# Kernel tuning notes

Measured on AMD Instinct MI355X. Metric: run time of the kernel, lower is better.

Reference implementation:

```python
import jax, jax.numpy as jnp
import numpy as np

HIDDEN = 1024
INTER = 4096
NUM_EXPERTS = 8
TOP_K = 2


def setup_inputs() -> dict:
    key = jax.random.key(0)
    k1, k2, k3, k4 = jax.random.split(key, 4)
    hidden_states = jax.random.normal(k1, (4, 1024, HIDDEN), dtype=jnp.float32)
    gate_w = jax.random.normal(k2, (HIDDEN, NUM_EXPERTS), dtype=jnp.float32) * 0.02
    w1 = jax.random.normal(k3, (NUM_EXPERTS, HIDDEN, INTER), dtype=jnp.float32) * 0.02
    w2 = jax.random.normal(k4, (NUM_EXPERTS, INTER, HIDDEN), dtype=jnp.float32) * 0.02
    return {"hidden_states": hidden_states, "gate_w": gate_w, "w1": w1, "w2": w2}


def reference(hidden_states, gate_w, w1, w2):
    B, S, H = hidden_states.shape
    x = hidden_states.reshape(-1, H)                       # [T, H]
    T = x.shape[0]
    router_logits = x @ gate_w                             # [T, E]
    probs = jax.nn.softmax(router_logits.astype(jnp.float32), axis=-1)
    routing_weights, selected_experts = jax.lax.top_k(probs, TOP_K)  # [T, K]
    routing_weights = routing_weights / routing_weights.sum(-1, keepdims=True)
    routing_weights = routing_weights.astype(x.dtype)
    # combine[t, e] = sum_k rw[t, k] * (sel[t, k] == e)
    combine = jnp.zeros((T, NUM_EXPERTS), x.dtype).at[
        jnp.arange(T)[:, None], selected_experts
    ].add(routing_weights)
    # dense grouped MLP over all experts; zero combine weight drops unrouted pairs
    h1 = jax.nn.gelu(jnp.einsum('th,ehi->tei', x, w1), approximate=False)  # [T, E, I]
    y = jnp.einsum('tei,eih->teh', h1, w2)                 # [T, E, H]
    out = jnp.einsum('teh,te->th', y, combine)             # [T, H]
    return out.reshape(B, S, H), router_logits
```

## Files before the change

### kernel.cpp

```cpp
#include <hip/hip_runtime.h>
#include <hip/hip_bf16.h>
#include <math.h>

typedef unsigned short u16;
typedef unsigned int u32;
typedef __bf16 bf16x8 __attribute__((ext_vector_type(8)));
typedef float f32x4 __attribute__((ext_vector_type(4)));

#define T_TOK 4096
#define HID   1024
#define INTER 4096
#define NEXP  8

#define WS_NEEDED 209978368ull

__device__ __forceinline__ u16 f2bf(float f) {
    u32 u = __builtin_bit_cast(u32, f);
    u += 0x7FFFu + ((u >> 16) & 1u);
    return (u16)(u >> 16);
}

__device__ __forceinline__ void gl2lds16(const void* g, void* l) {
    __builtin_amdgcn_global_load_lds(
        (const __attribute__((address_space(1))) u32*)g,
        (__attribute__((address_space(3))) u32*)l, 16, 0, 0);
}

__device__ __forceinline__ float fast_gelu(float v) {
    float u2 = v * (-1.5957691216f - 0.0713548163f * v * v);
    return v / (1.0f + __expf(u2));
}

__global__ __launch_bounds__(256) void router_kernel(
    const float* __restrict__ x, const float* __restrict__ gw,
    float* __restrict__ logits, int* __restrict__ counts,
    int* __restrict__ tlist, float* __restrict__ wlist)
{
    const int lane = threadIdx.x & 63, wv = threadIdx.x >> 6;
    const int t = blockIdx.x * 4 + wv;
    const float* xr = x + (size_t)t * HID;
    float a[8] = {0.f,0.f,0.f,0.f,0.f,0.f,0.f,0.f};
    for (int h = lane; h < HID; h += 64) {
        float xv = xr[h];
        const float4* g4 = (const float4*)(gw + h * 8);
        float4 g0 = g4[0], g1 = g4[1];
        a[0] += xv * g0.x; a[1] += xv * g0.y; a[2] += xv * g0.z; a[3] += xv * g0.w;
        a[4] += xv * g1.x; a[5] += xv * g1.y; a[6] += xv * g1.z; a[7] += xv * g1.w;
    }
#pragma unroll
    for (int e = 0; e < 8; e++) {
        float v = a[e];
        for (int o = 32; o > 0; o >>= 1) v += __shfl_down(v, o, 64);
        a[e] = v;
    }
    if (lane == 0) {
#pragma unroll
        for (int e = 0; e < 8; e++) logits[(size_t)t * 8 + e] = a[e];
        int e1 = 0; float b1 = a[0];
        for (int e = 1; e < 8; e++) if (a[e] > b1) { b1 = a[e]; e1 = e; }
        int e2 = -1; float b2 = -1e30f;
        for (int e = 0; e < 8; e++) if (e != e1 && a[e] > b2) { b2 = a[e]; e2 = e; }
        float wa = 1.0f / (1.0f + expf(b2 - b1));
        float wb = 1.0f - wa;
        int p = atomicAdd(&counts[e1], 1);
        tlist[e1 * T_TOK + p] = t; wlist[e1 * T_TOK + p] = wa;
        p = atomicAdd(&counts[e2], 1);
        tlist[e2 * T_TOK + p] = t; wlist[e2 * T_TOK + p] = wb;
    }
}

__global__ void scan_kernel(const int* __restrict__ counts, int* __restrict__ offs)
{
    if (threadIdx.x == 0) {
        int s = 0;
        for (int e = 0; e < 8; e++) { offs[e] = s; s += counts[e]; }
    }
}

__global__ __launch_bounds__(256) void convert_x_kernel(
    const float* __restrict__ src, u16* __restrict__ dst)
{
    const int idx = (blockIdx.x * 256 + threadIdx.x) * 8;
    float4 f0 = *(const float4*)(src + idx);
    float4 f1 = *(const float4*)(src + idx + 4);
    uint4 o;
    o.x = (u32)f2bf(f0.x) | ((u32)f2bf(f0.y) << 16);
    o.y = (u32)f2bf(f0.z) | ((u32)f2bf(f0.w) << 16);
    o.z = (u32)f2bf(f1.x) | ((u32)f2bf(f1.y) << 16);
    o.w = (u32)f2bf(f1.z) | ((u32)f2bf(f1.w) << 16);
    *(uint4*)(dst + idx) = o;
}

__global__ __launch_bounds__(256) void transpose_convert_kernel(
    const float* __restrict__ src, u16* __restrict__ dst, int R, int C)
{
    __shared__ float tl[64][65];
    const int e = blockIdx.z;
    const int c0 = blockIdx.x * 64, r0 = blockIdx.y * 64;
    const float* s = src + (size_t)e * R * C + (size_t)r0 * C + c0;
    const int tid = threadIdx.x;
#pragma unroll
    for (int it = 0; it < 4; it++) {
        int idx = it * 256 + tid;
        int r = idx >> 4;
        int c4 = (idx & 15) * 4;
        float4 v = *(const float4*)(s + (size_t)r * C + c4);
        tl[c4 + 0][r] = v.x;
        tl[c4 + 1][r] = v.y;
        tl[c4 + 2][r] = v.z;
        tl[c4 + 3][r] = v.w;
    }
    __syncthreads();
    u16* d = dst + (size_t)e * C * R + (size_t)c0 * R + r0;
#pragma unroll
    for (int it = 0; it < 2; it++) {
        int idx = it * 256 + tid;
        int c = idx >> 3;
        int rg = (idx & 7) * 8;
        u32 o[4];
#pragma unroll
        for (int p = 0; p < 4; p++)
            o[p] = (u32)f2bf(tl[c][rg + 2 * p]) | ((u32)f2bf(tl[c][rg + 2 * p + 1]) << 16);
        *(uint4*)(d + (size_t)c * R + rg) = *(uint4*)o;
    }
}

__global__ __launch_bounds__(256, 1) void gemm1_kernel(
    const u16* __restrict__ xb, const u16* __restrict__ w1t,
    const int* __restrict__ counts, const int* __restrict__ offs,
    const int* __restrict__ tlist, u16* __restrict__ h1b)
{
    const int e = blockIdx.z, mt = blockIdx.y, nt = blockIdx.x;
    const int cnt = counts[e];
    if (mt * 128 >= cnt) return;
    __shared__ __align__(16) u16 As[8192];
    __shared__ __align__(16) u16 Bs[8192];
    __shared__ int toks[128];
    const int tid = threadIdx.x, lane = tid & 63, wv = tid >> 6;
    if (tid < 128) toks[tid] = tlist[e * T_TOK + min(mt * 128 + tid, cnt - 1)];
    __syncthreads();

    f32x4 acc[4][4] = {};
    const int wm = wv & 1, wn = wv >> 1;
    const int sj = tid >> 3, sp = tid & 7;

    size_t abase[4], bbase[4];
    const u16* w1base = w1t + ((size_t)e * INTER + (size_t)nt * 128) * HID;
#pragma unroll
    for (int j = 0; j < 4; j++) {
        int m = j * 32 + sj;
        abase[j] = (size_t)toks[m] * HID + ((sp - m) & 7) * 8;
        bbase[j] = (size_t)m * HID + ((sp - m) & 7) * 8;
    }

    for (int h0 = 0; h0 < HID; h0 += 64) {
#pragma unroll
        for (int j = 0; j < 4; j++)
            gl2lds16(xb + abase[j] + h0, &As[j * 2048 + wv * 512]);
#pragma unroll
        for (int j = 0; j < 4; j++)
            gl2lds16(w1base + bbase[j] + h0, &Bs[j * 2048 + wv * 512]);
        __syncthreads();
#pragma unroll
        for (int kk = 0; kk < 2; kk++) {
            bf16x8 a[4], b[4];
            const int jjb = kk * 4 + (lane >> 4);
#pragma unroll
            for (int i = 0; i < 4; i++) {
                int m = wm * 64 + i * 16 + (lane & 15);
                a[i] = *(const bf16x8*)&As[m * 64 + ((jjb + m) & 7) * 8];
            }
#pragma unroll
            for (int i = 0; i < 4; i++) {
                int n = wn * 64 + i * 16 + (lane & 15);
                b[i] = *(const bf16x8*)&Bs[n * 64 + ((jjb + n) & 7) * 8];
            }
#pragma unroll
            for (int i = 0; i < 4; i++)
#pragma unroll
                for (int j = 0; j < 4; j++)
                    acc[i][j] = __builtin_amdgcn_mfma_f32_16x16x32_bf16(
                        a[i], b[j], acc[i][j], 0, 0, 0);
        }
        __syncthreads();
    }

    const int pb = offs[e] + mt * 128;
    const bool full = (mt * 128 + 128 <= cnt);
#pragma unroll
    for (int i = 0; i < 4; i++) {
        const int mb = wm * 64 + i * 16 + ((lane >> 4) << 2);
#pragma unroll
        for (int j = 0; j < 4; j++) {
            const int n = nt * 128 + wn * 64 + j * 16 + (lane & 15);
#pragma unroll
            for (int r = 0; r < 4; r++) {
                const int m = mb + r;
                if (full || mt * 128 + m < cnt) {
                    h1b[(size_t)(pb + m) * INTER + n] = f2bf(fast_gelu(acc[i][j][r]));
                }
            }
        }
    }
}

__global__ __launch_bounds__(256, 1) void gemm2_kernel(
    const u16* __restrict__ h1b, const u16* __restrict__ w2t,
    const int* __restrict__ counts, const int* __restrict__ offs,
    const int* __restrict__ tlist, const float* __restrict__ wlist,
    float* __restrict__ out)
{
    const int e = blockIdx.z, mt = blockIdx.y;
    const int nt = blockIdx.x & 7, ks = blockIdx.x >> 3;
    const int cnt = counts[e];
    if (mt * 128 >= cnt) return;
    __shared__ __align__(16) u16 As[8192];
    __shared__ __align__(16) u16 Bs[8192];
    __shared__ int toks[128];
    __shared__ float wgt[128];
    const int tid = threadIdx.x, lane = tid & 63, wv = tid >> 6;
    if (tid < 128) {
        int gi = e * T_TOK + min(mt * 128 + tid, cnt - 1);
        toks[tid] = tlist[gi];
        wgt[tid] = wlist[gi];
    }
    __syncthreads();

    f32x4 acc[4][4] = {};
    const int wm = wv & 1, wn = wv >> 1;
    const int sj = tid >> 3, sp = tid & 7;

    size_t abase[4], bbase[4];
    const u16* w2base = w2t + ((size_t)e * HID + (size_t)nt * 128) * INTER;
    const int prow = offs[e];
#pragma unroll
    for (int j = 0; j < 4; j++) {
        int m = j * 32 + sj;
        int row = prow + min(mt * 128 + m, cnt - 1);
        abase[j] = (size_t)row * INTER + ((sp - m) & 7) * 8;
        bbase[j] = (size_t)m * INTER + ((sp - m) & 7) * 8;
    }

    const int i_lo = ks * (INTER / 2), i_hi = i_lo + (INTER / 2);
    for (int i0 = i_lo; i0 < i_hi; i0 += 64) {
#pragma unroll
        for (int j = 0; j < 4; j++)
            gl2lds16(h1b + abase[j] + i0, &As[j * 2048 + wv * 512]);
#pragma unroll
        for (int j = 0; j < 4; j++)
            gl2lds16(w2base + bbase[j] + i0, &Bs[j * 2048 + wv * 512]);
        __syncthreads();
#pragma unroll
        for (int kk = 0; kk < 2; kk++) {
            bf16x8 a[4], b[4];
            const int jjb = kk * 4 + (lane >> 4);
#pragma unroll
            for (int i = 0; i < 4; i++) {
                int m = wm * 64 + i * 16 + (lane & 15);
                a[i] = *(const bf16x8*)&As[m * 64 + ((jjb + m) & 7) * 8];
            }
#pragma unroll
            for (int i = 0; i < 4; i++) {
                int n = wn * 64 + i * 16 + (lane & 15);
                b[i] = *(const bf16x8*)&Bs[n * 64 + ((jjb + n) & 7) * 8];
            }
#pragma unroll
            for (int i = 0; i < 4; i++)
#pragma unroll
                for (int j = 0; j < 4; j++)
                    acc[i][j] = __builtin_amdgcn_mfma_f32_16x16x32_bf16(
                        a[i], b[j], acc[i][j], 0, 0, 0);
        }
        __syncthreads();
    }

    const bool full = (mt * 128 + 128 <= cnt);
#pragma unroll
    for (int i = 0; i < 4; i++) {
        const int mb = wm * 64 + i * 16 + ((lane >> 4) << 2);
#pragma unroll
        for (int j = 0; j < 4; j++) {
            const int n = nt * 128 + wn * 64 + j * 16 + (lane & 15);
#pragma unroll
            for (int r = 0; r < 4; r++) {
                const int m = mb + r;
                if (full || mt * 128 + m < cnt) {
                    atomicAdd(&out[(size_t)toks[m] * HID + n], acc[i][j][r] * wgt[m]);
                }
            }
        }
    }
}

extern "C" void kernel_launch(void* const* d_in, const int* in_sizes, int n_in,
                              void* d_out, int out_size, void* d_ws, size_t ws_size,
                              hipStream_t stream)
{
    const float* x  = (const float*)d_in[0];
    const float* gw = (const float*)d_in[1];
    const float* w1 = (const float*)d_in[2];
    const float* w2 = (const float*)d_in[3];
    float* out    = (float*)d_out;
    float* logits = out + 4194304;

    char* ws = (char*)d_ws;
    int*   counts = (int*)ws;
    int*   offs   = (int*)(ws + 256);
    int*   tlist  = (int*)(ws + 1024);
    float* wlist  = (float*)(ws + 132096);
    u16*   xb     = (u16*)(ws + 263168);
    u16*   w1t    = (u16*)(ws + 8651776);
    u16*   w2t    = (u16*)(ws + 75760640);
    u16*   h1b    = (u16*)(ws + 142869504);

    if (ws_size < WS_NEEDED) return;

    hipMemsetAsync(out, 0, 4194304 * sizeof(float), stream);
    hipMemsetAsync(counts, 0, 256, stream);

    router_kernel<<<1024, 256, 0, stream>>>(x, gw, logits, counts, tlist, wlist);
    scan_kernel<<<1, 64, 0, stream>>>(counts, offs);
    convert_x_kernel<<<2048, 256, 0, stream>>>(x, xb);
    transpose_convert_kernel<<<dim3(64, 16, 8), 256, 0, stream>>>(w1, w1t, HID, INTER);
    transpose_convert_kernel<<<dim3(16, 64, 8), 256, 0, stream>>>(w2, w2t, INTER, HID);

    gemm1_kernel<<<dim3(32, 16, 8), 256, 0, stream>>>(xb, w1t, counts, offs, tlist, h1b);
    gemm2_kernel<<<dim3(16, 16, 8), 256, 0, stream>>>(h1b, w2t, counts, offs, tlist, wlist, out);
}
```

Baseline: 709.0 us.

## Use 256x256 tiles, 512-thread blocks and double-buffered LDS in expert GEMMs

Both expert GEMM kernels move from 128x128 tiles on 256 threads to 256x256 tiles on 512 threads, with each wave computing a 128x64 sub-tile. The goal is more data reuse per global load. LDS staging becomes double-buffered, so the next K-slice is loaded while the current one is computed, removing one barrier per iteration. The grid is flattened to 1D with expert index in the low bits, so blocks of different experts interleave. Offsets are also computed in 32-bit. In exchange the kernels use far more LDS (about 128KB) and registers, and fewer blocks run, which hurts load balance when experts are uneven.

```diff
diff --git a/kernel.cpp b/kernel.cpp
--- a/kernel.cpp
+++ b/kernel.cpp
@@ -125,168 +125,207 @@
     }
 }
 
-__global__ __launch_bounds__(256, 1) void gemm1_kernel(
+__global__ __launch_bounds__(512, 1) void gemm1_kernel(
     const u16* __restrict__ xb, const u16* __restrict__ w1t,
     const int* __restrict__ counts, const int* __restrict__ offs,
     const int* __restrict__ tlist, u16* __restrict__ h1b)
 {
-    const int e = blockIdx.z, mt = blockIdx.y, nt = blockIdx.x;
+    const int id = blockIdx.x;
+    const int e  = id & 7;
+    const int mt = (id >> 3) & 7;
+    const int nt = id >> 6;
     const int cnt = counts[e];
-    if (mt * 128 >= cnt) return;
-    __shared__ __align__(16) u16 As[8192];
-    __shared__ __align__(16) u16 Bs[8192];
-    __shared__ int toks[128];
+    if (mt * 256 >= cnt) return;
+
+    __shared__ __align__(16) u16 As[2][16384];
+    __shared__ __align__(16) u16 Bs[2][16384];
+    __shared__ int toks[256];
+
     const int tid = threadIdx.x, lane = tid & 63, wv = tid >> 6;
-    if (tid < 128) toks[tid] = tlist[e * T_TOK + min(mt * 128 + tid, cnt - 1)];
-    __syncthreads();
-
-    f32x4 acc[4][4] = {};
+    if (tid < 256) toks[tid] = tlist[e * T_TOK + min(mt * 256 + tid, cnt - 1)];
+    __syncthreads();
+
+    const int sr = tid >> 3;
+    const int sp = tid & 7;
+    u32 abase[4], bbase[4];
+    const u32 w1off = ((u32)e * INTER + (u32)nt * 256) * HID;
+#pragma unroll
+    for (int j = 0; j < 4; j++) {
+        int m = j * 64 + sr;
+        u32 rot = (u32)((sp - m) & 7) * 8;
+        abase[j] = (u32)toks[m] * HID + rot;
+        bbase[j] = w1off + (u32)m * HID + rot;
+    }
+
+    f32x4 acc[8][4] = {};
     const int wm = wv & 1, wn = wv >> 1;
-    const int sj = tid >> 3, sp = tid & 7;
-
-    size_t abase[4], bbase[4];
-    const u16* w1base = w1t + ((size_t)e * INTER + (size_t)nt * 128) * HID;
-#pragma unroll
-    for (int j = 0; j < 4; j++) {
-        int m = j * 32 + sj;
-        abase[j] = (size_t)toks[m] * HID + ((sp - m) & 7) * 8;
-        bbase[j] = (size_t)m * HID + ((sp - m) & 7) * 8;
-    }
-
-    for (int h0 = 0; h0 < HID; h0 += 64) {
+
+    auto STAGE = [&](int buf, int k0) {
 #pragma unroll
         for (int j = 0; j < 4; j++)
-            gl2lds16(xb + abase[j] + h0, &As[j * 2048 + wv * 512]);
+            gl2lds16(xb + abase[j] + k0, &As[buf][j * 4096 + wv * 512]);
 #pragma unroll
         for (int j = 0; j < 4; j++)
-            gl2lds16(w1base + bbase[j] + h0, &Bs[j * 2048 + wv * 512]);
-        __syncthreads();
+            gl2lds16(w1t + bbase[j] + k0, &Bs[buf][j * 4096 + wv * 512]);
+    };
+
+    auto COMPUTE = [&](int buf) {
 #pragma unroll
         for (int kk = 0; kk < 2; kk++) {
-            bf16x8 a[4], b[4];
+            bf16x8 a[8], b[4];
             const int jjb = kk * 4 + (lane >> 4);
 #pragma unroll
-            for (int i = 0; i < 4; i++) {
-                int m = wm * 64 + i * 16 + (lane & 15);
-                a[i] = *(const bf16x8*)&As[m * 64 + ((jjb + m) & 7) * 8];
-            }
-#pragma unroll
-            for (int i = 0; i < 4; i++) {
-                int n = wn * 64 + i * 16 + (lane & 15);
-                b[i] = *(const bf16x8*)&Bs[n * 64 + ((jjb + n) & 7) * 8];
-            }
-#pragma unroll
-            for (int i = 0; i < 4; i++)
+            for (int i = 0; i < 8; i++) {
+                int m = wm * 128 + i * 16 + (lane & 15);
+                a[i] = *(const bf16x8*)&As[buf][m * 64 + ((jjb + m) & 7) * 8];
+            }
+#pragma unroll
+            for (int j = 0; j < 4; j++) {
+                int n = wn * 64 + j * 16 + (lane & 15);
+                b[j] = *(const bf16x8*)&Bs[buf][n * 64 + ((jjb + n) & 7) * 8];
+            }
+#pragma unroll
+            for (int i = 0; i < 8; i++)
 #pragma unroll
                 for (int j = 0; j < 4; j++)
                     acc[i][j] = __builtin_amdgcn_mfma_f32_16x16x32_bf16(
                         a[i], b[j], acc[i][j], 0, 0, 0);
         }
+    };
+
+    STAGE(0, 0);
+    __syncthreads();
+    int cur = 0;
+#pragma unroll 1
+    for (int kt = 1; kt < HID / 64; kt++) {
+        STAGE(cur ^ 1, kt * 64);
+        COMPUTE(cur);
         __syncthreads();
-    }
-
-    const int pb = offs[e] + mt * 128;
-    const bool full = (mt * 128 + 128 <= cnt);
-#pragma unroll
-    for (int i = 0; i < 4; i++) {
-        const int mb = wm * 64 + i * 16 + ((lane >> 4) << 2);
+        cur ^= 1;
+    }
+    COMPUTE(cur);
+
+    const int pb = offs[e] + mt * 256;
+    const int rem = cnt - mt * 256;
+    const bool full = (rem >= 256);
+#pragma unroll
+    for (int i = 0; i < 8; i++) {
+        const int mb = wm * 128 + i * 16 + ((lane >> 4) << 2);
 #pragma unroll
         for (int j = 0; j < 4; j++) {
-            const int n = nt * 128 + wn * 64 + j * 16 + (lane & 15);
+            const int n = nt * 256 + wn * 64 + j * 16 + (lane & 15);
 #pragma unroll
             for (int r = 0; r < 4; r++) {
                 const int m = mb + r;
-                if (full || mt * 128 + m < cnt) {
+                if (full || m < rem)
                     h1b[(size_t)(pb + m) * INTER + n] = f2bf(fast_gelu(acc[i][j][r]));
-                }
             }
         }
     }
 }
 
-__global__ __launch_bounds__(256, 1) void gemm2_kernel(
+__global__ __launch_bounds__(512, 1) void gemm2_kernel(
     const u16* __restrict__ h1b, const u16* __restrict__ w2t,
     const int* __restrict__ counts, const int* __restrict__ offs,
     const int* __restrict__ tlist, const float* __restrict__ wlist,
     float* __restrict__ out)
 {
-    const int e = blockIdx.z, mt = blockIdx.y;
-    const int nt = blockIdx.x & 7, ks = blockIdx.x >> 3;
+    const int id = blockIdx.x;
+    const int e  = id & 7;
+    const int mt = (id >> 3) & 7;
+    const int nt = (id >> 6) & 3;
+    const int ks = id >> 8;
     const int cnt = counts[e];
-    if (mt * 128 >= cnt) return;
-    __shared__ __align__(16) u16 As[8192];
-    __shared__ __align__(16) u16 Bs[8192];
-    __shared__ int toks[128];
-    __shared__ float wgt[128];
+    if (mt * 256 >= cnt) return;
+
+    __shared__ __align__(16) u16 As[2][16384];
+    __shared__ __align__(16) u16 Bs[2][16384];
+    __shared__ int toks[256];
+    __shared__ float wgt[256];
+
     const int tid = threadIdx.x, lane = tid & 63, wv = tid >> 6;
-    if (tid < 128) {
-        int gi = e * T_TOK + min(mt * 128 + tid, cnt - 1);
+    if (tid < 256) {
+        int gi = e * T_TOK + min(mt * 256 + tid, cnt - 1);
         toks[tid] = tlist[gi];
-        wgt[tid] = wlist[gi];
-    }
-    __syncthreads();
-
-    f32x4 acc[4][4] = {};
+        wgt[tid]  = wlist[gi];
+    }
+    __syncthreads();
+
+    const int sr = tid >> 3;
+    const int sp = tid & 7;
+    u32 abase[4], bbase[4];
+    const int prow = offs[e];
+#pragma unroll
+    for (int j = 0; j < 4; j++) {
+        int m = j * 64 + sr;
+        u32 rot = (u32)((sp - m) & 7) * 8;
+        int row = prow + min(mt * 256 + m, cnt - 1);
+        abase[j] = (u32)row * INTER + rot;
+        bbase[j] = ((u32)e * HID + (u32)nt * 256 + (u32)m) * INTER + rot;
+    }
+
+    f32x4 acc[8][4] = {};
     const int wm = wv & 1, wn = wv >> 1;
-    const int sj = tid >> 3, sp = tid & 7;
-
-    size_t abase[4], bbase[4];
-    const u16* w2base = w2t + ((size_t)e * HID + (size_t)nt * 128) * INTER;
-    const int prow = offs[e];
-#pragma unroll
-    for (int j = 0; j < 4; j++) {
-        int m = j * 32 + sj;
-        int row = prow + min(mt * 128 + m, cnt - 1);
-        abase[j] = (size_t)row * INTER + ((sp - m) & 7) * 8;
-        bbase[j] = (size_t)m * INTER + ((sp - m) & 7) * 8;
-    }
-
-    const int i_lo = ks * (INTER / 2), i_hi = i_lo + (INTER / 2);
-    for (int i0 = i_lo; i0 < i_hi; i0 += 64) {
+
+    auto STAGE = [&](int buf, int k0) {
 #pragma unroll
         for (int j = 0; j < 4; j++)
-            gl2lds16(h1b + abase[j] + i0, &As[j * 2048 + wv * 512]);
+            gl2lds16(h1b + abase[j] + k0, &As[buf][j * 4096 + wv * 512]);
 #pragma unroll
         for (int j = 0; j < 4; j++)
-            gl2lds16(w2base + bbase[j] + i0, &Bs[j * 2048 + wv * 512]);
-        __syncthreads();
+            gl2lds16(w2t + bbase[j] + k0, &Bs[buf][j * 4096 + wv * 512]);
+    };
+
+    auto COMPUTE = [&](int buf) {
 #pragma unroll
         for (int kk = 0; kk < 2; kk++) {
-            bf16x8 a[4], b[4];
+            bf16x8 a[8], b[4];
             const int jjb = kk * 4 + (lane >> 4);
 #pragma unroll
-            for (int i = 0; i < 4; i++) {
-                int m = wm * 64 + i * 16 + (lane & 15);
-                a[i] = *(const bf16x8*)&As[m * 64 + ((jjb + m) & 7) * 8];
-            }
-#pragma unroll
-            for (int i = 0; i < 4; i++) {
-                int n = wn * 64 + i * 16 + (lane & 15);
-                b[i] = *(const bf16x8*)&Bs[n * 64 + ((jjb + n) & 7) * 8];
-            }
-#pragma unroll
-            for (int i = 0; i < 4; i++)
+            for (int i = 0; i < 8; i++) {
+                int m = wm * 128 + i * 16 + (lane & 15);
+                a[i] = *(const bf16x8*)&As[buf][m * 64 + ((jjb + m) & 7) * 8];
+            }
+#pragma unroll
+            for (int j = 0; j < 4; j++) {
+                int n = wn * 64 + j * 16 + (lane & 15);
+                b[j] = *(const bf16x8*)&Bs[buf][n * 64 + ((jjb + n) & 7) * 8];
+            }
+#pragma unroll
+            for (int i = 0; i < 8; i++)
 #pragma unroll
                 for (int j = 0; j < 4; j++)
                     acc[i][j] = __builtin_amdgcn_mfma_f32_16x16x32_bf16(
                         a[i], b[j], acc[i][j], 0, 0, 0);
         }
+    };
+
+    const u32 kbase = (u32)ks * (INTER / 2);
+    STAGE(0, kbase);
+    __syncthreads();
+    int cur = 0;
+#pragma unroll 1
+    for (int kt = 1; kt < (INTER / 2) / 64; kt++) {
+        STAGE(cur ^ 1, kbase + kt * 64);
+        COMPUTE(cur);
         __syncthreads();
-    }
-
-    const bool full = (mt * 128 + 128 <= cnt);
-#pragma unroll
-    for (int i = 0; i < 4; i++) {
-        const int mb = wm * 64 + i * 16 + ((lane >> 4) << 2);
+        cur ^= 1;
+    }
+    COMPUTE(cur);
+
+    const int rem = cnt - mt * 256;
+    const bool full = (rem >= 256);
+#pragma unroll
+    for (int i = 0; i < 8; i++) {
+        const int mb = wm * 128 + i * 16 + ((lane >> 4) << 2);
 #pragma unroll
         for (int j = 0; j < 4; j++) {
-            const int n = nt * 128 + wn * 64 + j * 16 + (lane & 15);
+            const int n = nt * 256 + wn * 64 + j * 16 + (lane & 15);
 #pragma unroll
             for (int r = 0; r < 4; r++) {
                 const int m = mb + r;
-                if (full || mt * 128 + m < cnt) {
+                if (full || m < rem)
                     atomicAdd(&out[(size_t)toks[m] * HID + n], acc[i][j][r] * wgt[m]);
-                }
             }
         }
     }
@@ -324,6 +363,6 @@
     transpose_convert_kernel<<<dim3(64, 16, 8), 256, 0, stream>>>(w1, w1t, HID, INTER);
     transpose_convert_kernel<<<dim3(16, 64, 8), 256, 0, stream>>>(w2, w2t, INTER, HID);
 
-    gemm1_kernel<<<dim3(32, 16, 8), 256, 0, stream>>>(xb, w1t, counts, offs, tlist, h1b);
-    gemm2_kernel<<<dim3(16, 16, 8), 256, 0, stream>>>(h1b, w2t, counts, offs, tlist, wlist, out);
-}
+    gemm1_kernel<<<1024, 512, 0, stream>>>(xb, w1t, counts, offs, tlist, h1b);
+    gemm2_kernel<<<512, 512, 0, stream>>>(h1b, w2t, counts, offs, tlist, wlist, out);
+}
```

Result: slower. 758.7 us (+7.0%).

## Replace LDS-staged GEMM tiles with direct global-to-register double-buffered loads

Applied to the files above, without the earlier changes.

Both expert GEMM kernels drop the shared-memory tiles filled through global_load_lds, along with the per-iteration barriers. Each wave now loads its MFMA fragments straight from global memory into registers and uses a two-stage register double buffer to overlap loads with MFMAs. The launch bound no longer forces one block per CU, and the grid order is swapped so the M-tile index varies fastest, which changes L2 reuse of weights. The cost is that each tile is fetched separately by every wave that uses it with no LDS sharing, which raises global/L2 traffic, and the 16-byte strided row loads may coalesce poorly.

```diff
diff --git a/kernel.cpp b/kernel.cpp
--- a/kernel.cpp
+++ b/kernel.cpp
@@ -18,12 +18,6 @@
     u32 u = __builtin_bit_cast(u32, f);
     u += 0x7FFFu + ((u >> 16) & 1u);
     return (u16)(u >> 16);
-}
-
-__device__ __forceinline__ void gl2lds16(const void* g, void* l) {
-    __builtin_amdgcn_global_load_lds(
-        (const __attribute__((address_space(1))) u32*)g,
-        (__attribute__((address_space(3))) u32*)l, 16, 0, 0);
 }
 
 __device__ __forceinline__ float fast_gelu(float v) {
@@ -125,68 +119,74 @@
     }
 }
 
-__global__ __launch_bounds__(256, 1) void gemm1_kernel(
+
+__global__ __launch_bounds__(256) void gemm1_kernel(
     const u16* __restrict__ xb, const u16* __restrict__ w1t,
     const int* __restrict__ counts, const int* __restrict__ offs,
     const int* __restrict__ tlist, u16* __restrict__ h1b)
 {
-    const int e = blockIdx.z, mt = blockIdx.y, nt = blockIdx.x;
+    const int mt = blockIdx.x, nt = blockIdx.y, e = blockIdx.z;
     const int cnt = counts[e];
     if (mt * 128 >= cnt) return;
-    __shared__ __align__(16) u16 As[8192];
-    __shared__ __align__(16) u16 Bs[8192];
+
     __shared__ int toks[128];
     const int tid = threadIdx.x, lane = tid & 63, wv = tid >> 6;
     if (tid < 128) toks[tid] = tlist[e * T_TOK + min(mt * 128 + tid, cnt - 1)];
     __syncthreads();
 
+    const int wm = wv & 1, wn = wv >> 1;
+    const int kq = (lane >> 4) * 8;
+
+    u32 aoff[4], boff[4];
+#pragma unroll
+    for (int i = 0; i < 4; i++) {
+        int m = wm * 64 + i * 16 + (lane & 15);
+        aoff[i] = (u32)toks[m] * HID + kq;
+    }
+#pragma unroll
+    for (int j = 0; j < 4; j++) {
+        int n = nt * 128 + wn * 64 + j * 16 + (lane & 15);
+        boff[j] = ((u32)e * INTER + (u32)n) * HID + kq;
+    }
+
     f32x4 acc[4][4] = {};
-    const int wm = wv & 1, wn = wv >> 1;
-    const int sj = tid >> 3, sp = tid & 7;
-
-    size_t abase[4], bbase[4];
-    const u16* w1base = w1t + ((size_t)e * INTER + (size_t)nt * 128) * HID;
-#pragma unroll
-    for (int j = 0; j < 4; j++) {
-        int m = j * 32 + sj;
-        abase[j] = (size_t)toks[m] * HID + ((sp - m) & 7) * 8;
-        bbase[j] = (size_t)m * HID + ((sp - m) & 7) * 8;
-    }
-
-    for (int h0 = 0; h0 < HID; h0 += 64) {
-#pragma unroll
-        for (int j = 0; j < 4; j++)
-            gl2lds16(xb + abase[j] + h0, &As[j * 2048 + wv * 512]);
-#pragma unroll
-        for (int j = 0; j < 4; j++)
-            gl2lds16(w1base + bbase[j] + h0, &Bs[j * 2048 + wv * 512]);
-        __syncthreads();
-#pragma unroll
-        for (int kk = 0; kk < 2; kk++) {
-            bf16x8 a[4], b[4];
-            const int jjb = kk * 4 + (lane >> 4);
-#pragma unroll
-            for (int i = 0; i < 4; i++) {
-                int m = wm * 64 + i * 16 + (lane & 15);
-                a[i] = *(const bf16x8*)&As[m * 64 + ((jjb + m) & 7) * 8];
-            }
-#pragma unroll
-            for (int i = 0; i < 4; i++) {
-                int n = wn * 64 + i * 16 + (lane & 15);
-                b[i] = *(const bf16x8*)&Bs[n * 64 + ((jjb + n) & 7) * 8];
-            }
-#pragma unroll
-            for (int i = 0; i < 4; i++)
-#pragma unroll
-                for (int j = 0; j < 4; j++)
-                    acc[i][j] = __builtin_amdgcn_mfma_f32_16x16x32_bf16(
-                        a[i], b[j], acc[i][j], 0, 0, 0);
+    bf16x8 a0[4], b0[4], a1[4], b1[4];
+
+#pragma unroll
+    for (int i = 0; i < 4; i++) a0[i] = *(const bf16x8*)(xb + aoff[i]);
+#pragma unroll
+    for (int j = 0; j < 4; j++) b0[j] = *(const bf16x8*)(w1t + boff[j]);
+
+    const int NT = HID / 32;
+#pragma unroll 1
+    for (int t = 0; t < NT; t += 2) {
+#pragma unroll
+        for (int i = 0; i < 4; i++) a1[i] = *(const bf16x8*)(xb + aoff[i] + (t + 1) * 32);
+#pragma unroll
+        for (int j = 0; j < 4; j++) b1[j] = *(const bf16x8*)(w1t + boff[j] + (t + 1) * 32);
+#pragma unroll
+        for (int i = 0; i < 4; i++)
+#pragma unroll
+            for (int j = 0; j < 4; j++)
+                acc[i][j] = __builtin_amdgcn_mfma_f32_16x16x32_bf16(
+                    a0[i], b0[j], acc[i][j], 0, 0, 0);
+        if (t + 2 < NT) {
+#pragma unroll
+            for (int i = 0; i < 4; i++) a0[i] = *(const bf16x8*)(xb + aoff[i] + (t + 2) * 32);
+#pragma unroll
+            for (int j = 0; j < 4; j++) b0[j] = *(const bf16x8*)(w1t + boff[j] + (t + 2) * 32);
         }
-        __syncthreads();
+#pragma unroll
+        for (int i = 0; i < 4; i++)
+#pragma unroll
+            for (int j = 0; j < 4; j++)
+                acc[i][j] = __builtin_amdgcn_mfma_f32_16x16x32_bf16(
+                    a1[i], b1[j], acc[i][j], 0, 0, 0);
     }
 
     const int pb = offs[e] + mt * 128;
-    const bool full = (mt * 128 + 128 <= cnt);
+    const int rem = cnt - mt * 128;
+    const bool full = (rem >= 128);
 #pragma unroll
     for (int i = 0; i < 4; i++) {
         const int mb = wm * 64 + i * 16 + ((lane >> 4) << 2);
@@ -196,85 +196,90 @@
 #pragma unroll
             for (int r = 0; r < 4; r++) {
                 const int m = mb + r;
-                if (full || mt * 128 + m < cnt) {
+                if (full || m < rem)
                     h1b[(size_t)(pb + m) * INTER + n] = f2bf(fast_gelu(acc[i][j][r]));
-                }
             }
         }
     }
 }
 
-__global__ __launch_bounds__(256, 1) void gemm2_kernel(
+__global__ __launch_bounds__(256) void gemm2_kernel(
     const u16* __restrict__ h1b, const u16* __restrict__ w2t,
     const int* __restrict__ counts, const int* __restrict__ offs,
     const int* __restrict__ tlist, const float* __restrict__ wlist,
     float* __restrict__ out)
 {
-    const int e = blockIdx.z, mt = blockIdx.y;
-    const int nt = blockIdx.x & 7, ks = blockIdx.x >> 3;
+    const int mt = blockIdx.x;
+    const int nt = blockIdx.y & 7, ks = blockIdx.y >> 3;
+    const int e = blockIdx.z;
     const int cnt = counts[e];
     if (mt * 128 >= cnt) return;
-    __shared__ __align__(16) u16 As[8192];
-    __shared__ __align__(16) u16 Bs[8192];
+
     __shared__ int toks[128];
     __shared__ float wgt[128];
     const int tid = threadIdx.x, lane = tid & 63, wv = tid >> 6;
     if (tid < 128) {
         int gi = e * T_TOK + min(mt * 128 + tid, cnt - 1);
         toks[tid] = tlist[gi];
-        wgt[tid] = wlist[gi];
+        wgt[tid]  = wlist[gi];
     }
     __syncthreads();
 
+    const int wm = wv & 1, wn = wv >> 1;
+    const int kq = (lane >> 4) * 8;
+    const u32 kbase = (u32)ks * (INTER / 2);
+    const int prow = offs[e];
+
+    u32 aoff[4], boff[4];
+#pragma unroll
+    for (int i = 0; i < 4; i++) {
+        int m = wm * 64 + i * 16 + (lane & 15);
+        int row = prow + min(mt * 128 + m, cnt - 1);
+        aoff[i] = (u32)row * INTER + kbase + kq;
+    }
+#pragma unroll
+    for (int j = 0; j < 4; j++) {
+        int n = nt * 128 + wn * 64 + j * 16 + (lane & 15);
+        boff[j] = ((u32)e * HID + (u32)n) * INTER + kbase + kq;
+    }
+
     f32x4 acc[4][4] = {};
-    const int wm = wv & 1, wn = wv >> 1;
-    const int sj = tid >> 3, sp = tid & 7;
-
-    size_t abase[4], bbase[4];
-    const u16* w2base = w2t + ((size_t)e * HID + (size_t)nt * 128) * INTER;
-    const int prow = offs[e];
-#pragma unroll
-    for (int j = 0; j < 4; j++) {
-        int m = j * 32 + sj;
-        int row = prow + min(mt * 128 + m, cnt - 1);
-        abase[j] = (size_t)row * INTER + ((sp - m) & 7) * 8;
-        bbase[j] = (size_t)m * INTER + ((sp - m) & 7) * 8;
-    }
-
-    const int i_lo = ks * (INTER / 2), i_hi = i_lo + (INTER / 2);
-    for (int i0 = i_lo; i0 < i_hi; i0 += 64) {
-#pragma unroll
-        for (int j = 0; j < 4; j++)
-            gl2lds16(h1b + abase[j] + i0, &As[j * 2048 + wv * 512]);
-#pragma unroll
-        for (int j = 0; j < 4; j++)
-            gl2lds16(w2base + bbase[j] + i0, &Bs[j * 2048 + wv * 512]);
-        __syncthreads();
-#pragma unroll
-        for (int kk = 0; kk < 2; kk++) {
-            bf16x8 a[4], b[4];
-            const int jjb = kk * 4 + (lane >> 4);
-#pragma unroll
-            for (int i = 0; i < 4; i++) {
-                int m = wm * 64 + i * 16 + (lane & 15);
-                a[i] = *(const bf16x8*)&As[m * 64 + ((jjb + m) & 7) * 8];
-            }
-#pragma unroll
-            for (int i = 0; i < 4; i++) {
-                int n = wn * 64 + i * 16 + (lane & 15);
-                b[i] = *(const bf16x8*)&Bs[n * 64 + ((jjb + n) & 7) * 8];
-            }
-#pragma unroll
-            for (int i = 0; i < 4; i++)
-#pragma unroll
-                for (int j = 0; j < 4; j++)
-                    acc[i][j] = __builtin_amdgcn_mfma_f32_16x16x32_bf16(
-                        a[i], b[j], acc[i][j], 0, 0, 0);
+    bf16x8 a0[4], b0[4], a1[4], b1[4];
+
+#pragma unroll
+    for (int i = 0; i < 4; i++) a0[i] = *(const bf16x8*)(h1b + aoff[i]);
+#pragma unroll
+    for (int j = 0; j < 4; j++) b0[j] = *(const bf16x8*)(w2t + boff[j]);
+
+    const int NT = (INTER / 2) / 32;
+#pragma unroll 1
+    for (int t = 0; t < NT; t += 2) {
+#pragma unroll
+        for (int i = 0; i < 4; i++) a1[i] = *(const bf16x8*)(h1b + aoff[i] + (t + 1) * 32);
+#pragma unroll
+        for (int j = 0; j < 4; j++) b1[j] = *(const bf16x8*)(w2t + boff[j] + (t + 1) * 32);
+#pragma unroll
+        for (int i = 0; i < 4; i++)
+#pragma unroll
+            for (int j = 0; j < 4; j++)
+                acc[i][j] = __builtin_amdgcn_mfma_f32_16x16x32_bf16(
+                    a0[i], b0[j], acc[i][j], 0, 0, 0);
+        if (t + 2 < NT) {
+#pragma unroll
+            for (int i = 0; i < 4; i++) a0[i] = *(const bf16x8*)(h1b + aoff[i] + (t + 2) * 32);
+#pragma unroll
+            for (int j = 0; j < 4; j++) b0[j] = *(const bf16x8*)(w2t + boff[j] + (t + 2) * 32);
         }
-        __syncthreads();
-    }
-
-    const bool full = (mt * 128 + 128 <= cnt);
+#pragma unroll
+        for (int i = 0; i < 4; i++)
+#pragma unroll
+            for (int j = 0; j < 4; j++)
+                acc[i][j] = __builtin_amdgcn_mfma_f32_16x16x32_bf16(
+                    a1[i], b1[j], acc[i][j], 0, 0, 0);
+    }
+
+    const int rem = cnt - mt * 128;
+    const bool full = (rem >= 128);
 #pragma unroll
     for (int i = 0; i < 4; i++) {
         const int mb = wm * 64 + i * 16 + ((lane >> 4) << 2);
@@ -284,9 +289,8 @@
 #pragma unroll
             for (int r = 0; r < 4; r++) {
                 const int m = mb + r;
-                if (full || mt * 128 + m < cnt) {
+                if (full || m < rem)
                     atomicAdd(&out[(size_t)toks[m] * HID + n], acc[i][j][r] * wgt[m]);
-                }
             }
         }
     }
@@ -324,6 +328,6 @@
     transpose_convert_kernel<<<dim3(64, 16, 8), 256, 0, stream>>>(w1, w1t, HID, INTER);
     transpose_convert_kernel<<<dim3(16, 64, 8), 256, 0, stream>>>(w2, w2t, INTER, HID);
 
-    gemm1_kernel<<<dim3(32, 16, 8), 256, 0, stream>>>(xb, w1t, counts, offs, tlist, h1b);
+    gemm1_kernel<<<dim3(16, 32, 8), 256, 0, stream>>>(xb, w1t, counts, offs, tlist, h1b);
     gemm2_kernel<<<dim3(16, 16, 8), 256, 0, stream>>>(h1b, w2t, counts, offs, tlist, wlist, out);
 }
```

New measurement: 1.361 ms. +92.0%, slower.

## Replace atomic scatter in gemm2 with split-K buffers and a combine kernel

Applied to the files above, without the earlier changes.

The x-to-bf16 conversion moves into the router kernel, and the scan kernel is removed by computing expert offsets inline from counts. gemm2 no longer does float atomicAdd into the output. It writes each split-K partial to a dense per-expert buffer that reuses the w1t region, and a new combine kernel gathers the two expert rows per token and applies the routing weights recomputed from the logits. This removes the output memset and atomic contention, at the cost of extra y buffer traffic and one more launch. It also drops two launches.

```diff
diff --git a/kernel.cpp b/kernel.cpp
--- a/kernel.cpp
+++ b/kernel.cpp
@@ -34,14 +34,16 @@
 __global__ __launch_bounds__(256) void router_kernel(
     const float* __restrict__ x, const float* __restrict__ gw,
     float* __restrict__ logits, int* __restrict__ counts,
-    int* __restrict__ tlist, float* __restrict__ wlist)
+    int* __restrict__ tlist, u32* __restrict__ sel, u16* __restrict__ xb)
 {
     const int lane = threadIdx.x & 63, wv = threadIdx.x >> 6;
     const int t = blockIdx.x * 4 + wv;
     const float* xr = x + (size_t)t * HID;
+    u16* xw = xb + (size_t)t * HID;
     float a[8] = {0.f,0.f,0.f,0.f,0.f,0.f,0.f,0.f};
     for (int h = lane; h < HID; h += 64) {
         float xv = xr[h];
+        xw[h] = f2bf(xv);
         const float4* g4 = (const float4*)(gw + h * 8);
         float4 g0 = g4[0], g1 = g4[1];
         a[0] += xv * g0.x; a[1] += xv * g0.y; a[2] += xv * g0.z; a[3] += xv * g0.w;
@@ -60,35 +62,13 @@
         for (int e = 1; e < 8; e++) if (a[e] > b1) { b1 = a[e]; e1 = e; }
         int e2 = -1; float b2 = -1e30f;
         for (int e = 0; e < 8; e++) if (e != e1 && a[e] > b2) { b2 = a[e]; e2 = e; }
-        float wa = 1.0f / (1.0f + expf(b2 - b1));
-        float wb = 1.0f - wa;
         int p = atomicAdd(&counts[e1], 1);
-        tlist[e1 * T_TOK + p] = t; wlist[e1 * T_TOK + p] = wa;
+        tlist[e1 * T_TOK + p] = t;
+        sel[2 * t + 0] = (u32)e1 | ((u32)p << 3);
         p = atomicAdd(&counts[e2], 1);
-        tlist[e2 * T_TOK + p] = t; wlist[e2 * T_TOK + p] = wb;
-    }
-}
-
-__global__ void scan_kernel(const int* __restrict__ counts, int* __restrict__ offs)
-{
-    if (threadIdx.x == 0) {
-        int s = 0;
-        for (int e = 0; e < 8; e++) { offs[e] = s; s += counts[e]; }
-    }
-}
-
-__global__ __launch_bounds__(256) void convert_x_kernel(
-    const float* __restrict__ src, u16* __restrict__ dst)
-{
-    const int idx = (blockIdx.x * 256 + threadIdx.x) * 8;
-    float4 f0 = *(const float4*)(src + idx);
-    float4 f1 = *(const float4*)(src + idx + 4);
-    uint4 o;
-    o.x = (u32)f2bf(f0.x) | ((u32)f2bf(f0.y) << 16);
-    o.y = (u32)f2bf(f0.z) | ((u32)f2bf(f0.w) << 16);
-    o.z = (u32)f2bf(f1.x) | ((u32)f2bf(f1.y) << 16);
-    o.w = (u32)f2bf(f1.z) | ((u32)f2bf(f1.w) << 16);
-    *(uint4*)(dst + idx) = o;
+        tlist[e2 * T_TOK + p] = t;
+        sel[2 * t + 1] = (u32)e2 | ((u32)p << 3);
+    }
 }
 
 __global__ __launch_bounds__(256) void transpose_convert_kernel(
@@ -127,8 +107,8 @@
 
 __global__ __launch_bounds__(256, 1) void gemm1_kernel(
     const u16* __restrict__ xb, const u16* __restrict__ w1t,
-    const int* __restrict__ counts, const int* __restrict__ offs,
-    const int* __restrict__ tlist, u16* __restrict__ h1b)
+    const int* __restrict__ counts, const int* __restrict__ tlist,
+    u16* __restrict__ h1b)
 {
     const int e = blockIdx.z, mt = blockIdx.y, nt = blockIdx.x;
     const int cnt = counts[e];
@@ -185,7 +165,10 @@
         __syncthreads();
     }
 
-    const int pb = offs[e] + mt * 128;
+    int prow = 0;
+#pragma unroll
+    for (int i = 0; i < 8; i++) prow += (i < e) ? counts[i] : 0;
+    const int pb = prow + mt * 128;
     const bool full = (mt * 128 + 128 <= cnt);
 #pragma unroll
     for (int i = 0; i < 4; i++) {
@@ -206,9 +189,8 @@
 
 __global__ __launch_bounds__(256, 1) void gemm2_kernel(
     const u16* __restrict__ h1b, const u16* __restrict__ w2t,
-    const int* __restrict__ counts, const int* __restrict__ offs,
-    const int* __restrict__ tlist, const float* __restrict__ wlist,
-    float* __restrict__ out)
+    const int* __restrict__ counts, const int* __restrict__ tlist,
+    float* __restrict__ y)
 {
     const int e = blockIdx.z, mt = blockIdx.y;
     const int nt = blockIdx.x & 7, ks = blockIdx.x >> 3;
@@ -216,15 +198,11 @@
     if (mt * 128 >= cnt) return;
     __shared__ __align__(16) u16 As[8192];
     __shared__ __align__(16) u16 Bs[8192];
-    __shared__ int toks[128];
-    __shared__ float wgt[128];
     const int tid = threadIdx.x, lane = tid & 63, wv = tid >> 6;
-    if (tid < 128) {
-        int gi = e * T_TOK + min(mt * 128 + tid, cnt - 1);
-        toks[tid] = tlist[gi];
-        wgt[tid] = wlist[gi];
-    }
-    __syncthreads();
+
+    int prow = 0;
+#pragma unroll
+    for (int i = 0; i < 8; i++) prow += (i < e) ? counts[i] : 0;
 
     f32x4 acc[4][4] = {};
     const int wm = wv & 1, wn = wv >> 1;
@@ -232,7 +210,6 @@
 
     size_t abase[4], bbase[4];
     const u16* w2base = w2t + ((size_t)e * HID + (size_t)nt * 128) * INTER;
-    const int prow = offs[e];
 #pragma unroll
     for (int j = 0; j < 4; j++) {
         int m = j * 32 + sj;
@@ -274,6 +251,7 @@
         __syncthreads();
     }
 
+    float* yk = y + (size_t)ks * (8192ull * HID);
     const bool full = (mt * 128 + 128 <= cnt);
 #pragma unroll
     for (int i = 0; i < 4; i++) {
@@ -285,11 +263,44 @@
             for (int r = 0; r < 4; r++) {
                 const int m = mb + r;
                 if (full || mt * 128 + m < cnt) {
-                    atomicAdd(&out[(size_t)toks[m] * HID + n], acc[i][j][r] * wgt[m]);
+                    yk[(size_t)(prow + mt * 128 + m) * HID + n] = acc[i][j][r];
                 }
             }
         }
     }
+}
+
+__global__ __launch_bounds__(256) void combine_kernel(
+    const float* __restrict__ y, const u32* __restrict__ sel,
+    const int* __restrict__ counts, const float* __restrict__ logits,
+    float* __restrict__ out)
+{
+    const int t = blockIdx.x;
+    const u32 s0 = sel[2 * t + 0], s1 = sel[2 * t + 1];
+    const int e0 = s0 & 7, p0 = s0 >> 3;
+    const int e1 = s1 & 7, p1 = s1 >> 3;
+    int off0 = 0, off1 = 0;
+#pragma unroll
+    for (int i = 0; i < 8; i++) {
+        int c = counts[i];
+        off0 += (i < e0) ? c : 0;
+        off1 += (i < e1) ? c : 0;
+    }
+    const size_t g0 = (size_t)(off0 + p0) * HID;
+    const size_t g1 = (size_t)(off1 + p1) * HID;
+    const float la = logits[(size_t)t * 8 + e0];
+    const float lb = logits[(size_t)t * 8 + e1];
+    const float w0 = 1.0f / (1.0f + expf(lb - la));
+    const float w1 = 1.0f - w0;
+
+    const int c = threadIdx.x * 4;
+    const float* y1p = y + 8192ull * HID;
+    f32x4 a0 = *(const f32x4*)(y + g0 + c);
+    f32x4 a1 = *(const f32x4*)(y1p + g0 + c);
+    f32x4 b0 = *(const f32x4*)(y + g1 + c);
+    f32x4 b1 = *(const f32x4*)(y1p + g1 + c);
+    f32x4 o = w0 * (a0 + a1) + w1 * (b0 + b1);
+    *(f32x4*)(out + (size_t)t * HID + c) = o;
 }
 
 extern "C" void kernel_launch(void* const* d_in, const int* in_sizes, int n_in,
@@ -305,25 +316,23 @@
 
     char* ws = (char*)d_ws;
     int*   counts = (int*)ws;
-    int*   offs   = (int*)(ws + 256);
     int*   tlist  = (int*)(ws + 1024);
-    float* wlist  = (float*)(ws + 132096);
+    u32*   sel    = (u32*)(ws + 132096);
     u16*   xb     = (u16*)(ws + 263168);
     u16*   w1t    = (u16*)(ws + 8651776);
+    float* y      = (float*)(ws + 8651776);
     u16*   w2t    = (u16*)(ws + 75760640);
     u16*   h1b    = (u16*)(ws + 142869504);
 
     if (ws_size < WS_NEEDED) return;
 
-    hipMemsetAsync(out, 0, 4194304 * sizeof(float), stream);
     hipMemsetAsync(counts, 0, 256, stream);
 
-    router_kernel<<<1024, 256, 0, stream>>>(x, gw, logits, counts, tlist, wlist);
-    scan_kernel<<<1, 64, 0, stream>>>(counts, offs);
-    convert_x_kernel<<<2048, 256, 0, stream>>>(x, xb);
+    router_kernel<<<1024, 256, 0, stream>>>(x, gw, logits, counts, tlist, sel, xb);
     transpose_convert_kernel<<<dim3(64, 16, 8), 256, 0, stream>>>(w1, w1t, HID, INTER);
     transpose_convert_kernel<<<dim3(16, 64, 8), 256, 0, stream>>>(w2, w2t, INTER, HID);
 
-    gemm1_kernel<<<dim3(32, 16, 8), 256, 0, stream>>>(xb, w1t, counts, offs, tlist, h1b);
-    gemm2_kernel<<<dim3(16, 16, 8), 256, 0, stream>>>(h1b, w2t, counts, offs, tlist, wlist, out);
-}
+    gemm1_kernel<<<dim3(32, 16, 8), 256, 0, stream>>>(xb, w1t, counts, tlist, h1b);
+    gemm2_kernel<<<dim3(16, 16, 8), 256, 0, stream>>>(h1b, w2t, counts, tlist, y);
+    combine_kernel<<<T_TOK, 256, 0, stream>>>(y, sel, counts, logits, out);
+}
```

New measurement: 683.3 us. -3.6%, faster.
